# Optimization experiments

Measured on AMD Instinct MI355X. Metric: run time of the kernel, lower is better.

Reference implementation:

```python
import jax, jax.numpy as jnp
import numpy as np

N_NODES = 50000
N_EDGES = 1600000
IN_FEATS = 128
HIDDEN = 16
HEADS = 8
SLOPE = 0.2


def setup_inputs() -> dict:
    key = jax.random.key(0)
    ks = jax.random.split(key, 9)
    feat = jax.random.normal(ks[0], (N_NODES, IN_FEATS), dtype=jnp.float32)
    edge_src = jax.random.randint(ks[1], (N_EDGES,), 0, N_NODES, dtype=jnp.int32)
    edge_dst = jax.random.randint(ks[2], (N_EDGES,), 0, N_NODES, dtype=jnp.int32)
    # layer 0: in=128 -> H*F=128 ; layer 1: in=128 (concat of layer 0) -> 128
    s0 = 1.0 / np.sqrt(IN_FEATS)
    W0 = jax.random.normal(ks[3], (IN_FEATS, HEADS * HIDDEN), dtype=jnp.float32) * s0
    al0 = jax.random.normal(ks[4], (HEADS, HIDDEN), dtype=jnp.float32) * 0.1
    ar0 = jax.random.normal(ks[5], (HEADS, HIDDEN), dtype=jnp.float32) * 0.1
    W1 = jax.random.normal(ks[6], (HEADS * HIDDEN, HEADS * HIDDEN), dtype=jnp.float32) * s0
    al1 = jax.random.normal(ks[7], (HEADS, HIDDEN), dtype=jnp.float32) * 0.1
    ar1 = jax.random.normal(ks[8], (HEADS, HIDDEN), dtype=jnp.float32) * 0.1
    return {"feat": feat, "edge_src": edge_src, "edge_dst": edge_dst,
            "W0": W0, "al0": al0, "ar0": ar0, "W1": W1, "al1": al1, "ar1": ar1}


def _gat_conv(feat, W, al, ar, src, dst):
    """One DGL-style GATConv: no bias, no residual, no dropout, no activation."""
    n = feat.shape[0]
    h = (feat @ W).reshape(n, HEADS, HIDDEN)              # [N,H,F]
    el = jnp.sum(h * al, axis=-1)                          # [N,H]
    er = jnp.sum(h * ar, axis=-1)                          # [N,H]
    e = jax.nn.leaky_relu(el[src] + er[dst], negative_slope=SLOPE)  # [E,H]
    # edge softmax over incoming edges of each dst node
    m = jax.ops.segment_max(e, dst, num_segments=n)        # [N,H]
    ex = jnp.exp(e - m[dst])                               # [E,H]
    denom = jax.ops.segment_sum(ex, dst, num_segments=n)   # [N,H]
    alpha = ex / jnp.where(denom[dst] > 0, denom[dst], 1.0)
    # message passing: gather src features, weight, scatter-add to dst
    out = jax.ops.segment_sum(h[src] * alpha[:, :, None], dst, num_segments=n)
    return out                                             # [N,H,F]


def reference(feat, edge_src, edge_dst, W0, al0, ar0, W1, al1, ar1):
    n = feat.shape[0]
    # step 1 + concat (flatten heads)
    x = _gat_conv(feat, W0, al0, ar0, edge_src, edge_dst).reshape(n, HEADS * HIDDEN)
    # step 2 + concat
    x = _gat_conv(x, W1, al1, ar1, edge_src, edge_dst).reshape(n, HEADS * HIDDEN)
    return x
```

## Files before the change

kernel.cpp:

```cpp
#include <hip/hip_runtime.h>
#include <hip/hip_bf16.h>


#define HEADS 8
#define HID 16
#define HF 128
#define SLOPE 0.2f

#define BSHIFT 8
#define BRANGE 256
#define CHUNK 4096

typedef __attribute__((ext_vector_type(8))) short bf16x8;
typedef __attribute__((ext_vector_type(4))) float f32x4;

static __device__ __forceinline__ unsigned int f2bf(float f) {
    unsigned int u = __float_as_uint(f);
    u += 0x7fffu + ((u >> 16) & 1u);
    return u >> 16;
}


__global__ __launch_bounds__(512) void bucket_hist_kernel(
    const int* __restrict__ dst, int* __restrict__ bcount, int E, int nb) {
    __shared__ int h[BRANGE];
    int t = threadIdx.x;
    if (t < BRANGE) h[t] = 0;
    __syncthreads();
    int base = blockIdx.x * CHUNK;
    int end = base + CHUNK; if (end > E) end = E;
    for (int i = base + t; i < end; i += 512)
        atomicAdd(&h[dst[i] >> BSHIFT], 1);
    __syncthreads();
    if (t < nb && h[t]) atomicAdd(&bcount[t], h[t]);
}

__global__ __launch_bounds__(256) void bucket_scan_kernel(
    const int* __restrict__ bcount, int* __restrict__ bbase,
    int* __restrict__ gcur, int* __restrict__ rowptr, int nb, int N, int E) {
    __shared__ int s[256];
    int t = threadIdx.x;
    s[t] = (t < nb) ? bcount[t] : 0;
    __syncthreads();
    #pragma unroll
    for (int off = 1; off < 256; off <<= 1) {
        int v = (t >= off) ? s[t - off] : 0;
        __syncthreads();
        s[t] += v;
        __syncthreads();
    }
    int excl = (t == 0) ? 0 : s[t - 1];
    if (t < nb) { bbase[t] = excl; gcur[t] = excl; }
    if (t == 0) { bbase[nb] = E; rowptr[N] = E; }
}

__global__ __launch_bounds__(512) void bucket_scatter_kernel(
    const int* __restrict__ src, const int* __restrict__ dst,
    int* __restrict__ gcur, int* __restrict__ stage, int E, int nb) {
    __shared__ int hist[BRANGE];
    __shared__ int lscan[BRANGE];
    __shared__ int lcur[BRANGE];
    __shared__ int boff[BRANGE];
    __shared__ int sstage[CHUNK];
    int t = threadIdx.x;
    if (t < BRANGE) hist[t] = 0;
    __syncthreads();
    int base = blockIdx.x * CHUNK;
    int end = base + CHUNK; if (end > E) end = E;

    for (int i = base + t; i < end; i += 512)
        atomicAdd(&hist[dst[i] >> BSHIFT], 1);
    __syncthreads();

    if (t < 256) lscan[t] = hist[t];
    __syncthreads();
    #pragma unroll
    for (int off = 1; off < 256; off <<= 1) {
        int v = 0;
        if (t < 256 && t >= off) v = lscan[t - off];
        __syncthreads();
        if (t < 256) lscan[t] += v;
        __syncthreads();
    }
    int ex = 0;
    if (t < 256) ex = (t == 0) ? 0 : lscan[t - 1];
    __syncthreads();
    if (t < 256) {
        lcur[t] = ex;
        lscan[t] = ex;
        if (t < nb && hist[t] > 0) boff[t] = atomicAdd(&gcur[t], hist[t]);
    }
    __syncthreads();

    for (int i = base + t; i < end; i += 512) {
        int d = dst[i];
        int b = d >> BSHIFT;
        int pos = atomicAdd(&lcur[b], 1);
        sstage[pos] = (src[i] & 0xFFFF) | ((d & (BRANGE - 1)) << 16) | (b << 24);
    }
    __syncthreads();

    int total = end - base;
    for (int i = t; i < total; i += 512) {
        int p = sstage[i];
        int b = ((unsigned)p) >> 24;
        int gpos = boff[b] + (i - lscan[b]);
        stage[gpos] = p;
    }
}

__global__ __launch_bounds__(512) void bucket_csr_kernel(
    const int* __restrict__ stage, const int* __restrict__ bbase,
    int* __restrict__ rowptr, unsigned short* __restrict__ col, int N, int nb) {
    __shared__ int hist[BRANGE];
    __shared__ int lscan[BRANGE];
    __shared__ int lcur[BRANGE];
    int b = blockIdx.x;
    int t = threadIdx.x;
    int e0 = bbase[b], e1 = bbase[b + 1];
    if (t < BRANGE) hist[t] = 0;
    __syncthreads();
    for (int i = e0 + t; i < e1; i += 512)
        atomicAdd(&hist[(stage[i] >> 16) & (BRANGE - 1)], 1);
    __syncthreads();
    if (t < 256) lscan[t] = hist[t];
    __syncthreads();
    #pragma unroll
    for (int off = 1; off < 256; off <<= 1) {
        int v = 0;
        if (t < 256 && t >= off) v = lscan[t - off];
        __syncthreads();
        if (t < 256) lscan[t] += v;
        __syncthreads();
    }
    if (t < 256) {
        int ex = (t == 0) ? 0 : lscan[t - 1];
        lcur[t] = ex;
        int node = (b << BSHIFT) + t;
        if (node < N) rowptr[node] = e0 + ex;
    }
    __syncthreads();
    for (int i = e0 + t; i < e1; i += 512) {
        int p = stage[i];
        int pos = e0 + atomicAdd(&lcur[(p >> 16) & (BRANGE - 1)], 1);
        col[pos] = (unsigned short)(p & 0xFFFF);
    }
}


__global__ __launch_bounds__(256) void wtrans_kernel(const float* __restrict__ W,
                                                     unsigned short* __restrict__ Wtb) {
    int gid = blockIdx.x * 256 + threadIdx.x;
    int c = gid >> 3;
    int k0 = (gid & 7) * 16;
    #pragma unroll
    for (int q = 0; q < 4; ++q) {
        int k = k0 + q * 4;
        ushort4 o = make_ushort4(
            (unsigned short)f2bf(W[(k + 0) * HF + c]),
            (unsigned short)f2bf(W[(k + 1) * HF + c]),
            (unsigned short)f2bf(W[(k + 2) * HF + c]),
            (unsigned short)f2bf(W[(k + 3) * HF + c]));
        *(ushort4*)(Wtb + (size_t)c * HF + k) = o;
    }
}


__global__ __launch_bounds__(256) void gemm_mfma_kernel(
    const float* __restrict__ X, const unsigned short* __restrict__ Wtb,
    const float* __restrict__ AL, const float* __restrict__ AR,
    unsigned short* __restrict__ Hb, float* __restrict__ EL,
    float* __restrict__ ER, int n) {
    __shared__ __align__(16) unsigned short xs[64 * HF];
    __shared__ __align__(16) unsigned short ws[HF * HF];
    int t = threadIdx.x;
    int row0 = blockIdx.x * 64;

    {
        int r = t >> 2;
        int k0 = (t & 3) * 32;
        int gr = row0 + r;
        float4 f[8];
        if (gr < n) {
            const float4* p = (const float4*)(X + (size_t)gr * HF + k0);
            #pragma unroll
            for (int i = 0; i < 8; ++i) f[i] = p[i];
        } else {
            #pragma unroll
            for (int i = 0; i < 8; ++i) f[i] = make_float4(0.f, 0.f, 0.f, 0.f);
        }
        unsigned int rowbase = r * 256;
        unsigned int sw = (r & 7) << 4;
        #pragma unroll
        for (int g2 = 0; g2 < 4; ++g2) {
            float4 a = f[g2 * 2], b = f[g2 * 2 + 1];
            int4 pk;
            pk.x = (int)(f2bf(a.x) | (f2bf(a.y) << 16));
            pk.y = (int)(f2bf(a.z) | (f2bf(a.w) << 16));
            pk.z = (int)(f2bf(b.x) | (f2bf(b.y) << 16));
            pk.w = (int)(f2bf(b.z) | (f2bf(b.w) << 16));
            unsigned int addr = rowbase + ((unsigned)((k0 + g2 * 8) * 2) ^ sw);
            *(int4*)((char*)xs + addr) = pk;
        }
    }
    {
        int c = t >> 1;
        unsigned int kb0 = (t & 1) * 128;
        const int4* src = (const int4*)((const char*)Wtb + (size_t)c * 256 + kb0);
        unsigned int sw = (c & 7) << 4;
        #pragma unroll
        for (int i = 0; i < 8; ++i) {
            int4 v = src[i];
            unsigned int addr = c * 256 + ((kb0 + i * 16) ^ sw);
            *(int4*)((char*)ws + addr) = v;
        }
    }
    __syncthreads();

    int wv = t >> 6;
    int l = t & 63;
    int lr = l & 15;
    int g = l >> 4;

    bf16x8 bfr[4];
    {
        int r = wv * 16 + lr;
        unsigned int rowbase = r * 256;
        unsigned int sw = (r & 7) << 4;
        #pragma unroll
        for (int s = 0; s < 4; ++s) {
            unsigned int kbyte = (unsigned)((s * 32 + g * 8) * 2);
            bfr[s] = *(bf16x8*)((char*)xs + rowbase + (kbyte ^ sw));
        }
    }

    f32x4 acc[8];
    #pragma unroll
    for (int ct = 0; ct < 8; ++ct) acc[ct] = (f32x4){0.f, 0.f, 0.f, 0.f};

    #pragma unroll
    for (int ct = 0; ct < 8; ++ct) {
        int c = ct * 16 + lr;
        unsigned int rowbase = c * 256;
        unsigned int sw = (c & 7) << 4;
        #pragma unroll
        for (int s = 0; s < 4; ++s) {
            unsigned int kbyte = (unsigned)((s * 32 + g * 8) * 2);
            bf16x8 af = *(bf16x8*)((char*)ws + rowbase + (kbyte ^ sw));
            acc[ct] = __builtin_amdgcn_mfma_f32_16x16x32_bf16(af, bfr[s], acc[ct], 0, 0, 0);
        }
    }

    int grow = row0 + wv * 16 + lr;
    bool valid = grow < n;

    if (valid) {
        #pragma unroll
        for (int ct = 0; ct < 8; ++ct) {
            ushort4 hb4 = make_ushort4(
                (unsigned short)f2bf(acc[ct][0]), (unsigned short)f2bf(acc[ct][1]),
                (unsigned short)f2bf(acc[ct][2]), (unsigned short)f2bf(acc[ct][3]));
            *(ushort4*)(Hb + (size_t)grow * HF + ct * 16 + g * 4) = hb4;
        }
    }

    #pragma unroll
    for (int ct = 0; ct < 8; ++ct) {
        float e1 = 0.f, e2 = 0.f;
        #pragma unroll
        for (int rg = 0; rg < 4; ++rg) {
            float alv = AL[ct * 16 + g * 4 + rg];
            float arv = AR[ct * 16 + g * 4 + rg];
            e1 += acc[ct][rg] * alv;
            e2 += acc[ct][rg] * arv;
        }
        e1 += __shfl_xor(e1, 16); e1 += __shfl_xor(e1, 32);
        e2 += __shfl_xor(e2, 16); e2 += __shfl_xor(e2, 32);
        if (g == 0 && valid) {
            EL[grow * HEADS + ct] = e1;
            ER[grow * HEADS + ct] = e2;
        }
    }
}


__global__ __launch_bounds__(256) void gat_aggregate_kernel(
    const unsigned int* __restrict__ HbU,
    const float* __restrict__ EL, const float* __restrict__ ER,
    const int* __restrict__ rowptr, const unsigned short* __restrict__ col,
    float* __restrict__ OUT, int n) {
    int wid = (int)((blockIdx.x * blockDim.x + threadIdx.x) >> 6);
    if (wid >= n) return;
    int lane = threadIdx.x & 63;
    int s0 = rowptr[wid], s1 = rowptr[wid + 1];
    size_t ob = (size_t)wid * HF;
    if (s1 == s0) {
        ((float2*)(OUT + ob))[lane] = make_float2(0.f, 0.f);
        return;
    }

    int h = lane & 7;
    int j = lane >> 3;
    int hC = lane >> 3;
    float er_h = ER[wid * HEADS + h];

    float accx = 0.f, accy = 0.f;
    float dpart = 0.f;

    for (int base = s0; base < s1; base += 8) {
        int i = base + j;
        int icl = i < s1 ? i : s1 - 1;
        int sj = (int)col[icl];
        float e = EL[sj * HEADS + h] + er_h;
        e = fmaxf(e, SLOPE * e);
        float w = __expf(e);
        if (i >= s1) w = 0.f;
        dpart += w;

        if (base + 8 <= s1) {
            #pragma unroll
            for (int jj = 0; jj < 8; ++jj) {
                float wC = __shfl(w, jj * 8 + hC);
                int s = __builtin_amdgcn_readlane(sj, jj * 8);
                unsigned int pv = HbU[(size_t)s * 64 + lane];
                accx += wC * __uint_as_float(pv << 16);
                accy += wC * __uint_as_float(pv & 0xffff0000u);
            }
        } else {
            int ne = s1 - base;
            for (int jj = 0; jj < ne; ++jj) {
                float wC = __shfl(w, jj * 8 + hC);
                int s = __builtin_amdgcn_readlane(sj, jj * 8);
                unsigned int pv = HbU[(size_t)s * 64 + lane];
                accx += wC * __uint_as_float(pv << 16);
                accy += wC * __uint_as_float(pv & 0xffff0000u);
            }
        }
    }

    dpart += __shfl_xor(dpart, 8);
    dpart += __shfl_xor(dpart, 16);
    dpart += __shfl_xor(dpart, 32);
    float rC = 1.f / __shfl(dpart, hC);

    ((float2*)(OUT + ob))[lane] = make_float2(accx * rC, accy * rC);
}


extern "C" void kernel_launch(void* const* d_in, const int* in_sizes, int n_in,
                              void* d_out, int out_size, void* d_ws, size_t ws_size,
                              hipStream_t stream) {
    const float* feat = (const float*)d_in[0];
    const int*   esrc = (const int*)d_in[1];
    const int*   edst = (const int*)d_in[2];
    const float* W0   = (const float*)d_in[3];
    const float* al0  = (const float*)d_in[4];
    const float* ar0  = (const float*)d_in[5];
    const float* W1   = (const float*)d_in[6];
    const float* al1  = (const float*)d_in[7];
    const float* ar1  = (const float*)d_in[8];
    float* out = (float*)d_out;

    const int N = in_sizes[0] / HF;
    const int E = in_sizes[1];
    const int nb = (N + BRANGE - 1) >> BSHIFT;

    char* w = (char*)d_ws;
    auto alloc = [&](size_t bytes) -> void* {
        void* p = (void*)w;
        w += (bytes + 255) & ~(size_t)255;
        return p;
    };
    unsigned short* hb   = (unsigned short*)alloc((size_t)N * HF * 2);
    float* x1     = (float*)alloc((size_t)N * HF * 4);
    float* el_buf = (float*)alloc((size_t)N * HEADS * 4);
    float* er_buf = (float*)alloc((size_t)N * HEADS * 4);
    int*   rowptr = (int*)alloc((size_t)(N + 1) * 4);
    unsigned short* col = (unsigned short*)alloc((size_t)E * 2);
    int*   bcount = (int*)alloc((size_t)nb * 4);
    int*   bbase  = (int*)alloc((size_t)(nb + 1) * 4);
    int*   gcur   = (int*)alloc((size_t)nb * 4);
    unsigned short* wtb0 = (unsigned short*)alloc((size_t)HF * HF * 2);
    unsigned short* wtb1 = (unsigned short*)alloc((size_t)HF * HF * 2);
    int*   stage  = (int*)x1;

    wtrans_kernel<<<4, 256, 0, stream>>>(W0, wtb0);
    wtrans_kernel<<<4, 256, 0, stream>>>(W1, wtb1);

    hipMemsetAsync(bcount, 0, (size_t)nb * 4, stream);
    int gChunk = (E + CHUNK - 1) / CHUNK;
    bucket_hist_kernel<<<gChunk, 512, 0, stream>>>(edst, bcount, E, nb);
    bucket_scan_kernel<<<1, 256, 0, stream>>>(bcount, bbase, gcur, rowptr, nb, N, E);
    bucket_scatter_kernel<<<gChunk, 512, 0, stream>>>(esrc, edst, gcur, stage, E, nb);
    bucket_csr_kernel<<<nb, 512, 0, stream>>>(stage, bbase, rowptr, col, N, nb);

    int gGemm = (N + 63) / 64;
    int gAgg  = (N * 64 + 255) / 256;

    gemm_mfma_kernel<<<gGemm, 256, 0, stream>>>(feat, wtb0, al0, ar0, hb, el_buf, er_buf, N);
    gat_aggregate_kernel<<<gAgg, 256, 0, stream>>>((const unsigned int*)hb, el_buf, er_buf,
                                                   rowptr, col, x1, N);

    gemm_mfma_kernel<<<gGemm, 256, 0, stream>>>(x1, wtb1, al1, ar1, hb, el_buf, er_buf, N);
    gat_aggregate_kernel<<<gAgg, 256, 0, stream>>>((const unsigned int*)hb, el_buf, er_buf,
                                                   rowptr, col, out, N);
}
```

Baseline: 231.9 us.

## Use deterministic two-level bucket scan and bf16 intermediate layer output

Bucket offsets are now computed from a per-block histogram matrix with a two-stage scan, rather than global atomics plus a re-histogram in the scatter pass. This makes the scatter deterministic and drops one read of dst. The layer-0 aggregate now writes bf16 instead of fp32, and the layer-1 GEMM reads it directly, which halves that intermediate traffic and skips the conversion. The cost is extra scan kernels and a separate stage buffer.

```diff
diff --git a/kernel.cpp b/kernel.cpp
--- a/kernel.cpp
+++ b/kernel.cpp
@@ -21,8 +21,8 @@
 }
 
 
-__global__ __launch_bounds__(512) void bucket_hist_kernel(
-    const int* __restrict__ dst, int* __restrict__ bcount, int E, int nb) {
+__global__ __launch_bounds__(512) void bhist_kernel(
+    const int* __restrict__ dst, int* __restrict__ bhistT, int E, int nb, int nblk) {
     __shared__ int h[BRANGE];
     int t = threadIdx.x;
     if (t < BRANGE) h[t] = 0;
@@ -32,15 +32,36 @@
     for (int i = base + t; i < end; i += 512)
         atomicAdd(&h[dst[i] >> BSHIFT], 1);
     __syncthreads();
-    if (t < nb && h[t]) atomicAdd(&bcount[t], h[t]);
-}
-
-__global__ __launch_bounds__(256) void bucket_scan_kernel(
-    const int* __restrict__ bcount, int* __restrict__ bbase,
-    int* __restrict__ gcur, int* __restrict__ rowptr, int nb, int N, int E) {
+    if (t < nb) bhistT[(size_t)t * nblk + blockIdx.x] = h[t];
+}
+
+__global__ __launch_bounds__(64) void bscan1_kernel(
+    const int* __restrict__ bhistT, int* __restrict__ boffT,
+    int* __restrict__ btot, int nblk) {
+    int b = blockIdx.x;
+    int l = threadIdx.x;
+    int carry = 0;
+    for (int c0 = 0; c0 < nblk; c0 += 64) {
+        int blk = c0 + l;
+        int v = (blk < nblk) ? bhistT[(size_t)b * nblk + blk] : 0;
+        int x = v;
+        #pragma unroll
+        for (int off = 1; off < 64; off <<= 1) {
+            int y = __shfl_up(x, off, 64);
+            if (l >= off) x += y;
+        }
+        if (blk < nblk) boffT[(size_t)b * nblk + blk] = carry + x - v;
+        carry += __shfl(x, 63);
+    }
+    if (l == 0) btot[b] = carry;
+}
+
+__global__ __launch_bounds__(256) void bscan2_kernel(
+    const int* __restrict__ btot, int* __restrict__ bbase,
+    int* __restrict__ rowptr, int nb, int N, int E) {
     __shared__ int s[256];
     int t = threadIdx.x;
-    s[t] = (t < nb) ? bcount[t] : 0;
+    s[t] = (t < nb) ? btot[t] : 0;
     __syncthreads();
     #pragma unroll
     for (int off = 1; off < 256; off <<= 1) {
@@ -50,29 +71,25 @@
         __syncthreads();
     }
     int excl = (t == 0) ? 0 : s[t - 1];
-    if (t < nb) { bbase[t] = excl; gcur[t] = excl; }
+    if (t < nb) bbase[t] = excl;
     if (t == 0) { bbase[nb] = E; rowptr[N] = E; }
 }
 
 __global__ __launch_bounds__(512) void bucket_scatter_kernel(
     const int* __restrict__ src, const int* __restrict__ dst,
-    int* __restrict__ gcur, int* __restrict__ stage, int E, int nb) {
-    __shared__ int hist[BRANGE];
+    const int* __restrict__ bhistT, const int* __restrict__ boffT,
+    const int* __restrict__ bbase, int* __restrict__ stage,
+    int E, int nb, int nblk) {
     __shared__ int lscan[BRANGE];
     __shared__ int lcur[BRANGE];
-    __shared__ int boff[BRANGE];
+    __shared__ int gbase[BRANGE];
     __shared__ int sstage[CHUNK];
     int t = threadIdx.x;
-    if (t < BRANGE) hist[t] = 0;
-    __syncthreads();
-    int base = blockIdx.x * CHUNK;
+    int blk = blockIdx.x;
+    int base = blk * CHUNK;
     int end = base + CHUNK; if (end > E) end = E;
 
-    for (int i = base + t; i < end; i += 512)
-        atomicAdd(&hist[dst[i] >> BSHIFT], 1);
-    __syncthreads();
-
-    if (t < 256) lscan[t] = hist[t];
+    if (t < 256) lscan[t] = (t < nb) ? bhistT[(size_t)t * nblk + blk] : 0;
     __syncthreads();
     #pragma unroll
     for (int off = 1; off < 256; off <<= 1) {
@@ -88,7 +105,7 @@
     if (t < 256) {
         lcur[t] = ex;
         lscan[t] = ex;
-        if (t < nb && hist[t] > 0) boff[t] = atomicAdd(&gcur[t], hist[t]);
+        if (t < nb) gbase[t] = bbase[t] + boffT[(size_t)t * nblk + blk];
     }
     __syncthreads();
 
@@ -104,7 +121,7 @@
     for (int i = t; i < total; i += 512) {
         int p = sstage[i];
         int b = ((unsigned)p) >> 24;
-        int gpos = boff[b] + (i - lscan[b]);
+        int gpos = gbase[b] + (i - lscan[b]);
         stage[gpos] = p;
     }
 }
@@ -166,8 +183,9 @@
 }
 
 
+template <bool XBF16>
 __global__ __launch_bounds__(256) void gemm_mfma_kernel(
-    const float* __restrict__ X, const unsigned short* __restrict__ Wtb,
+    const void* __restrict__ Xv, const unsigned short* __restrict__ Wtb,
     const float* __restrict__ AL, const float* __restrict__ AR,
     unsigned short* __restrict__ Hb, float* __restrict__ EL,
     float* __restrict__ ER, int n) {
@@ -178,29 +196,40 @@
 
     {
         int r = t >> 2;
-        int k0 = (t & 3) * 32;
         int gr = row0 + r;
-        float4 f[8];
-        if (gr < n) {
-            const float4* p = (const float4*)(X + (size_t)gr * HF + k0);
-            #pragma unroll
-            for (int i = 0; i < 8; ++i) f[i] = p[i];
-        } else {
-            #pragma unroll
-            for (int i = 0; i < 8; ++i) f[i] = make_float4(0.f, 0.f, 0.f, 0.f);
-        }
         unsigned int rowbase = r * 256;
         unsigned int sw = (r & 7) << 4;
-        #pragma unroll
-        for (int g2 = 0; g2 < 4; ++g2) {
-            float4 a = f[g2 * 2], b = f[g2 * 2 + 1];
-            int4 pk;
-            pk.x = (int)(f2bf(a.x) | (f2bf(a.y) << 16));
-            pk.y = (int)(f2bf(a.z) | (f2bf(a.w) << 16));
-            pk.z = (int)(f2bf(b.x) | (f2bf(b.y) << 16));
-            pk.w = (int)(f2bf(b.z) | (f2bf(b.w) << 16));
-            unsigned int addr = rowbase + ((unsigned)((k0 + g2 * 8) * 2) ^ sw);
-            *(int4*)((char*)xs + addr) = pk;
+        if (XBF16) {
+            unsigned int kb0 = (t & 3) * 64;
+            const char* src = (const char*)Xv + (size_t)gr * 256 + kb0;
+            #pragma unroll
+            for (int i = 0; i < 4; ++i) {
+                int4 v = (gr < n) ? *(const int4*)(src + i * 16)
+                                  : make_int4(0, 0, 0, 0);
+                *(int4*)((char*)xs + rowbase + ((kb0 + i * 16) ^ sw)) = v;
+            }
+        } else {
+            int k0 = (t & 3) * 32;
+            float4 f[8];
+            if (gr < n) {
+                const float4* p = (const float4*)((const float*)Xv + (size_t)gr * HF + k0);
+                #pragma unroll
+                for (int i = 0; i < 8; ++i) f[i] = p[i];
+            } else {
+                #pragma unroll
+                for (int i = 0; i < 8; ++i) f[i] = make_float4(0.f, 0.f, 0.f, 0.f);
+            }
+            #pragma unroll
+            for (int g2 = 0; g2 < 4; ++g2) {
+                float4 a = f[g2 * 2], b = f[g2 * 2 + 1];
+                int4 pk;
+                pk.x = (int)(f2bf(a.x) | (f2bf(a.y) << 16));
+                pk.y = (int)(f2bf(a.z) | (f2bf(a.w) << 16));
+                pk.z = (int)(f2bf(b.x) | (f2bf(b.y) << 16));
+                pk.w = (int)(f2bf(b.z) | (f2bf(b.w) << 16));
+                unsigned int addr = rowbase + ((unsigned)((k0 + g2 * 8) * 2) ^ sw);
+                *(int4*)((char*)xs + addr) = pk;
+            }
         }
     }
     {
@@ -284,18 +313,19 @@
 }
 
 
+template <bool OBF16>
 __global__ __launch_bounds__(256) void gat_aggregate_kernel(
     const unsigned int* __restrict__ HbU,
     const float* __restrict__ EL, const float* __restrict__ ER,
     const int* __restrict__ rowptr, const unsigned short* __restrict__ col,
-    float* __restrict__ OUT, int n) {
+    void* __restrict__ OUT, int n) {
     int wid = (int)((blockIdx.x * blockDim.x + threadIdx.x) >> 6);
     if (wid >= n) return;
     int lane = threadIdx.x & 63;
     int s0 = rowptr[wid], s1 = rowptr[wid + 1];
-    size_t ob = (size_t)wid * HF;
     if (s1 == s0) {
-        ((float2*)(OUT + ob))[lane] = make_float2(0.f, 0.f);
+        if (OBF16) ((unsigned int*)OUT)[(size_t)wid * 64 + lane] = 0u;
+        else ((float2*)OUT)[(size_t)wid * 64 + lane] = make_float2(0.f, 0.f);
         return;
     }
 
@@ -343,7 +373,12 @@
     dpart += __shfl_xor(dpart, 32);
     float rC = 1.f / __shfl(dpart, hC);
 
-    ((float2*)(OUT + ob))[lane] = make_float2(accx * rC, accy * rC);
+    if (OBF16) {
+        unsigned int o = f2bf(accx * rC) | (f2bf(accy * rC) << 16);
+        ((unsigned int*)OUT)[(size_t)wid * 64 + lane] = o;
+    } else {
+        ((float2*)OUT)[(size_t)wid * 64 + lane] = make_float2(accx * rC, accy * rC);
+    }
 }
 
 
@@ -364,6 +399,7 @@
     const int N = in_sizes[0] / HF;
     const int E = in_sizes[1];
     const int nb = (N + BRANGE - 1) >> BSHIFT;
+    const int nblk = (E + CHUNK - 1) / CHUNK;
 
     char* w = (char*)d_ws;
     auto alloc = [&](size_t bytes) -> void* {
@@ -372,36 +408,39 @@
         return p;
     };
     unsigned short* hb   = (unsigned short*)alloc((size_t)N * HF * 2);
-    float* x1     = (float*)alloc((size_t)N * HF * 4);
+    unsigned short* x1b  = (unsigned short*)alloc((size_t)N * HF * 2);
     float* el_buf = (float*)alloc((size_t)N * HEADS * 4);
     float* er_buf = (float*)alloc((size_t)N * HEADS * 4);
     int*   rowptr = (int*)alloc((size_t)(N + 1) * 4);
     unsigned short* col = (unsigned short*)alloc((size_t)E * 2);
-    int*   bcount = (int*)alloc((size_t)nb * 4);
+    int*   bhistT = (int*)alloc((size_t)nb * nblk * 4);
+    int*   boffT  = (int*)alloc((size_t)nb * nblk * 4);
+    int*   btot   = (int*)alloc((size_t)nb * 4);
     int*   bbase  = (int*)alloc((size_t)(nb + 1) * 4);
-    int*   gcur   = (int*)alloc((size_t)nb * 4);
     unsigned short* wtb0 = (unsigned short*)alloc((size_t)HF * HF * 2);
     unsigned short* wtb1 = (unsigned short*)alloc((size_t)HF * HF * 2);
-    int*   stage  = (int*)x1;
+    int*   stage  = (int*)alloc((size_t)E * 4);
 
     wtrans_kernel<<<4, 256, 0, stream>>>(W0, wtb0);
     wtrans_kernel<<<4, 256, 0, stream>>>(W1, wtb1);
 
-    hipMemsetAsync(bcount, 0, (size_t)nb * 4, stream);
-    int gChunk = (E + CHUNK - 1) / CHUNK;
-    bucket_hist_kernel<<<gChunk, 512, 0, stream>>>(edst, bcount, E, nb);
-    bucket_scan_kernel<<<1, 256, 0, stream>>>(bcount, bbase, gcur, rowptr, nb, N, E);
-    bucket_scatter_kernel<<<gChunk, 512, 0, stream>>>(esrc, edst, gcur, stage, E, nb);
+    bhist_kernel<<<nblk, 512, 0, stream>>>(edst, bhistT, E, nb, nblk);
+    bscan1_kernel<<<nb, 64, 0, stream>>>(bhistT, boffT, btot, nblk);
+    bscan2_kernel<<<1, 256, 0, stream>>>(btot, bbase, rowptr, nb, N, E);
+    bucket_scatter_kernel<<<nblk, 512, 0, stream>>>(esrc, edst, bhistT, boffT,
+                                                    bbase, stage, E, nb, nblk);
     bucket_csr_kernel<<<nb, 512, 0, stream>>>(stage, bbase, rowptr, col, N, nb);
 
     int gGemm = (N + 63) / 64;
     int gAgg  = (N * 64 + 255) / 256;
 
-    gemm_mfma_kernel<<<gGemm, 256, 0, stream>>>(feat, wtb0, al0, ar0, hb, el_buf, er_buf, N);
-    gat_aggregate_kernel<<<gAgg, 256, 0, stream>>>((const unsigned int*)hb, el_buf, er_buf,
-                                                   rowptr, col, x1, N);
-
-    gemm_mfma_kernel<<<gGemm, 256, 0, stream>>>(x1, wtb1, al1, ar1, hb, el_buf, er_buf, N);
-    gat_aggregate_kernel<<<gAgg, 256, 0, stream>>>((const unsigned int*)hb, el_buf, er_buf,
-                                                   rowptr, col, out, N);
-}
+    gemm_mfma_kernel<false><<<gGemm, 256, 0, stream>>>(feat, wtb0, al0, ar0,
+                                                       hb, el_buf, er_buf, N);
+    gat_aggregate_kernel<true><<<gAgg, 256, 0, stream>>>(
+        (const unsigned int*)hb, el_buf, er_buf, rowptr, col, x1b, N);
+
+    gemm_mfma_kernel<true><<<gGemm, 256, 0, stream>>>(x1b, wtb1, al1, ar1,
+                                                      hb, el_buf, er_buf, N);
+    gat_aggregate_kernel<false><<<gAgg, 256, 0, stream>>>(
+        (const unsigned int*)hb, el_buf, er_buf, rowptr, col, out, N);
+}
```

Measured after the change: 222.6 us. 4.0% less time.
